# Optimization experiments

Hardware: AMD Instinct MI355X
Metric: run time of the kernel (lower is better)

## Reference

```python
import jax, jax.numpy as jnp
from jax import lax
import numpy as np


def setup_inputs() -> dict:
    key = jax.random.key(0)
    kx, = jax.random.split(key, 1)
    B, T = 4096, 4096
    x = jax.random.normal(kx, (B, T), dtype=jnp.float32)
    omega_log = jnp.asarray(0.0, dtype=jnp.float32)
    alpha_log = jnp.asarray(0.0, dtype=jnp.float32)
    beta_log = jnp.asarray(0.0, dtype=jnp.float32)
    return {"x": x, "omega_log": omega_log, "alpha_log": alpha_log, "beta_log": beta_log}


def reference(x, omega_log, alpha_log, beta_log):
    # x: [B, T]
    ea = jnp.exp(alpha_log)
    eb = jnp.exp(beta_log)
    denom = 1.0 + ea + eb
    omega = jnp.exp(omega_log)
    alpha = ea / denom
    beta = eb / denom

    # initial variance: unbiased sample variance over time (torch.var default ddof=1)
    s0 = jnp.var(x, axis=1, ddof=1)  # [B]

    xsq = jnp.swapaxes(x[:, :-1] ** 2, 0, 1)  # [T-1, B]

    def step(s_prev, x2_t):
        s_t = omega + alpha * x2_t + beta * s_prev
        return s_t, s_t

    _, rest = lax.scan(step, s0, xsq)  # rest: [T-1, B]
    sigma2 = jnp.concatenate([s0[None, :], rest], axis=0)  # [T, B]
    return jnp.sqrt(jnp.swapaxes(sigma2, 0, 1))  # [B, T]
```

## Files before the change

kernel.cpp:

```cpp
#include <hip/hip_runtime.h>
#include <math.h>

#define B_ROWS 4096
#define T_COLS 4096
#define NTHREADS 256
#define CHUNK 16
#define NWAVES (NTHREADS / 64)

__device__ __forceinline__ int paddr(int e) { return e + (e >> 4); }
#define LDS_FLOATS (T_COLS + (T_COLS >> 4))

__global__ __launch_bounds__(NTHREADS) void garch_fused(
    const float* __restrict__ x,
    const float* __restrict__ p_omega_log,
    const float* __restrict__ p_alpha_log,
    const float* __restrict__ p_beta_log,
    float* __restrict__ out)
{
    __shared__ float lds[LDS_FLOATS];
    __shared__ float wA[NWAVES], wB[NWAVES];
    __shared__ float rSum[NWAVES], rSsq[NWAVES];

    const int t    = threadIdx.x;
    const int lane = t & 63;
    const int wv   = t >> 6;
    const int row  = blockIdx.x;
    const long rbase = (long)row * T_COLS;

    float ea = expf(p_alpha_log[0]);
    float eb = expf(p_beta_log[0]);
    float denom = 1.0f + ea + eb;
    float omega = expf(p_omega_log[0]);
    float alpha = ea / denom;
    float beta  = eb / denom;
    float b2 = beta * beta, b4 = b2 * b2, b8 = b4 * b4, b16 = b8 * b8;

    const float4* xv = reinterpret_cast<const float4*>(x + rbase);
#pragma unroll
    for (int k = 0; k < 4; ++k) {
        int e4 = k * 1024 + 4 * t;
        float4 v = xv[k * 256 + t];
        int a0 = paddr(e4);
        lds[a0 + 0] = v.x; lds[a0 + 1] = v.y; lds[a0 + 2] = v.z; lds[a0 + 3] = v.w;
    }
    __syncthreads();

    float xr[CHUNK];
    int cbase = 17 * t;
#pragma unroll
    for (int i = 0; i < CHUNK; ++i) xr[i] = lds[cbase + i];
    float prev = (t > 0) ? lds[paddr(CHUNK * t - 1)] : 0.0f;

    float sum = 0.0f, ssq = 0.0f;
#pragma unroll
    for (int i = 0; i < CHUNK; ++i) { sum += xr[i]; ssq = fmaf(xr[i], xr[i], ssq); }

    float bpart = 0.0f;
    if (t > 0) bpart = fmaf(alpha, prev * prev, omega);
#pragma unroll
    for (int i = 0; i < CHUNK - 1; ++i)
        bpart = fmaf(beta, bpart, fmaf(alpha, xr[i] * xr[i], omega));
    float apart = (t == 0) ? (b8 * b4 * b2 * beta) : b16;

    float s1 = sum, s2 = ssq;
#pragma unroll
    for (int d = 32; d > 0; d >>= 1) {
        s1 += __shfl_xor(s1, d);
        s2 += __shfl_xor(s2, d);
    }
    if (lane == 0) { rSum[wv] = s1; rSsq[wv] = s2; }
    __syncthreads();
    float tsum = rSum[0] + rSum[1] + rSum[2] + rSum[3];
    float tssq = rSsq[0] + rSsq[1] + rSsq[2] + rSsq[3];
    float s0 = (tssq - tsum * tsum * (1.0f / T_COLS)) * (1.0f / (T_COLS - 1));
    s0 = fmaxf(s0, 0.0f);

    float ia = apart, ib = bpart;
#pragma unroll
    for (int d = 1; d < 64; d <<= 1) {
        float pa = __shfl_up(ia, d);
        float pb = __shfl_up(ib, d);
        if (lane >= d) { ib = fmaf(ia, pb, ib); ia = ia * pa; }
    }
    if (lane == 63) { wA[wv] = ia; wB[wv] = ib; }
    __syncthreads();
    float sw = s0;
#pragma unroll
    for (int w = 0; w < NWAVES - 1; ++w)
        if (w < wv) sw = fmaf(wA[w], sw, wB[w]);
    float ea_ = __shfl_up(ia, 1);
    float eb_ = __shfl_up(ib, 1);
    if (lane == 0) { ea_ = 1.0f; eb_ = 0.0f; }
    float s = fmaf(ea_, sw, eb_);

    if (t == 0) {
        lds[cbase] = sqrtf(s);
#pragma unroll
        for (int i = 0; i < CHUNK - 1; ++i) {
            s = fmaf(beta, s, fmaf(alpha, xr[i] * xr[i], omega));
            lds[cbase + 1 + i] = sqrtf(s);
        }
    } else {
        s = fmaf(beta, s, fmaf(alpha, prev * prev, omega));
        lds[cbase] = sqrtf(s);
#pragma unroll
        for (int i = 0; i < CHUNK - 1; ++i) {
            s = fmaf(beta, s, fmaf(alpha, xr[i] * xr[i], omega));
            lds[cbase + 1 + i] = sqrtf(s);
        }
    }
    __syncthreads();

    float4* ov = reinterpret_cast<float4*>(out + rbase);
#pragma unroll
    for (int k = 0; k < 4; ++k) {
        int e4 = k * 1024 + 4 * t;
        int a0 = paddr(e4);
        float4 v;
        v.x = lds[a0 + 0]; v.y = lds[a0 + 1]; v.z = lds[a0 + 2]; v.w = lds[a0 + 3];
        ov[k * 256 + t] = v;
    }
}

extern "C" void kernel_launch(void* const* d_in, const int* in_sizes, int n_in,
                              void* d_out, int out_size, void* d_ws, size_t ws_size,
                              hipStream_t stream) {
    const float* x         = (const float*)d_in[0];
    const float* omega_log = (const float*)d_in[1];
    const float* alpha_log = (const float*)d_in[2];
    const float* beta_log  = (const float*)d_in[3];
    float* out = (float*)d_out;

    garch_fused<<<B_ROWS, NTHREADS, 0, stream>>>(x, omega_log, alpha_log, beta_log, out);
}
```

Measured before the change: 115.5 us.

## Load and store row chunks directly per thread, dropping LDS staging

Each thread now loads its 16 contiguous elements straight from global memory as four float4s and writes its outputs the same way, removing the LDS transpose buffer and two block barriers. The neighbouring element comes from a wave shuffle, with a scalar global load at wave boundaries. The two reductions now share one barrier, and sqrt uses the hardware builtin. The cost is strided per-thread accesses (64 bytes per thread per row chunk), which coalesce less cleanly than the original lane-contiguous float4 pattern.

```diff
diff --git a/kernel.cpp b/kernel.cpp
--- a/kernel.cpp
+++ b/kernel.cpp
@@ -7,9 +7,6 @@
 #define CHUNK 16
 #define NWAVES (NTHREADS / 64)
 
-__device__ __forceinline__ int paddr(int e) { return e + (e >> 4); }
-#define LDS_FLOATS (T_COLS + (T_COLS >> 4))
-
 __global__ __launch_bounds__(NTHREADS) void garch_fused(
     const float* __restrict__ x,
     const float* __restrict__ p_omega_log,
@@ -17,15 +14,12 @@
     const float* __restrict__ p_beta_log,
     float* __restrict__ out)
 {
-    __shared__ float lds[LDS_FLOATS];
-    __shared__ float wA[NWAVES], wB[NWAVES];
-    __shared__ float rSum[NWAVES], rSsq[NWAVES];
+    __shared__ float wA[NWAVES], wB[NWAVES], rSum[NWAVES], rSsq[NWAVES];
 
     const int t    = threadIdx.x;
     const int lane = t & 63;
     const int wv   = t >> 6;
-    const int row  = blockIdx.x;
-    const long rbase = (long)row * T_COLS;
+    const long rbase = (long)blockIdx.x * T_COLS;
 
     float ea = expf(p_alpha_log[0]);
     float eb = expf(p_beta_log[0]);
@@ -35,21 +29,13 @@
     float beta  = eb / denom;
     float b2 = beta * beta, b4 = b2 * b2, b8 = b4 * b4, b16 = b8 * b8;
 
-    const float4* xv = reinterpret_cast<const float4*>(x + rbase);
-#pragma unroll
-    for (int k = 0; k < 4; ++k) {
-        int e4 = k * 1024 + 4 * t;
-        float4 v = xv[k * 256 + t];
-        int a0 = paddr(e4);
-        lds[a0 + 0] = v.x; lds[a0 + 1] = v.y; lds[a0 + 2] = v.z; lds[a0 + 3] = v.w;
-    }
-    __syncthreads();
+    const float4* xv = reinterpret_cast<const float4*>(x + rbase + (long)CHUNK * t);
+    float4 v0 = xv[0], v1 = xv[1], v2 = xv[2], v3 = xv[3];
+    float xr[CHUNK] = { v0.x, v0.y, v0.z, v0.w,  v1.x, v1.y, v1.z, v1.w,
+                        v2.x, v2.y, v2.z, v2.w,  v3.x, v3.y, v3.z, v3.w };
 
-    float xr[CHUNK];
-    int cbase = 17 * t;
-#pragma unroll
-    for (int i = 0; i < CHUNK; ++i) xr[i] = lds[cbase + i];
-    float prev = (t > 0) ? lds[paddr(CHUNK * t - 1)] : 0.0f;
+    float prev = __shfl_up(xr[CHUNK - 1], 1);
+    if (lane == 0) prev = (t > 0) ? x[rbase + (long)CHUNK * t - 1] : 0.0f;
 
     float sum = 0.0f, ssq = 0.0f;
 #pragma unroll
@@ -68,12 +54,6 @@
         s1 += __shfl_xor(s1, d);
         s2 += __shfl_xor(s2, d);
     }
-    if (lane == 0) { rSum[wv] = s1; rSsq[wv] = s2; }
-    __syncthreads();
-    float tsum = rSum[0] + rSum[1] + rSum[2] + rSum[3];
-    float tssq = rSsq[0] + rSsq[1] + rSsq[2] + rSsq[3];
-    float s0 = (tssq - tsum * tsum * (1.0f / T_COLS)) * (1.0f / (T_COLS - 1));
-    s0 = fmaxf(s0, 0.0f);
 
     float ia = apart, ib = bpart;
 #pragma unroll
@@ -82,44 +62,49 @@
         float pb = __shfl_up(ib, d);
         if (lane >= d) { ib = fmaf(ia, pb, ib); ia = ia * pa; }
     }
-    if (lane == 63) { wA[wv] = ia; wB[wv] = ib; }
+
+    if (lane == 0)  { rSum[wv] = s1; rSsq[wv] = s2; }
+    if (lane == 63) { wA[wv] = ia;   wB[wv] = ib;  }
     __syncthreads();
+
+    float tsum = rSum[0] + rSum[1] + rSum[2] + rSum[3];
+    float tssq = rSsq[0] + rSsq[1] + rSsq[2] + rSsq[3];
+    float s0 = (tssq - tsum * tsum * (1.0f / T_COLS)) * (1.0f / (T_COLS - 1));
+    s0 = fmaxf(s0, 0.0f);
+
     float sw = s0;
 #pragma unroll
     for (int w = 0; w < NWAVES - 1; ++w)
         if (w < wv) sw = fmaf(wA[w], sw, wB[w]);
+
     float ea_ = __shfl_up(ia, 1);
     float eb_ = __shfl_up(ib, 1);
     if (lane == 0) { ea_ = 1.0f; eb_ = 0.0f; }
     float s = fmaf(ea_, sw, eb_);
 
+    float o[CHUNK];
     if (t == 0) {
-        lds[cbase] = sqrtf(s);
+        o[0] = __builtin_amdgcn_sqrtf(s);
 #pragma unroll
         for (int i = 0; i < CHUNK - 1; ++i) {
             s = fmaf(beta, s, fmaf(alpha, xr[i] * xr[i], omega));
-            lds[cbase + 1 + i] = sqrtf(s);
+            o[1 + i] = __builtin_amdgcn_sqrtf(s);
         }
     } else {
         s = fmaf(beta, s, fmaf(alpha, prev * prev, omega));
-        lds[cbase] = sqrtf(s);
+        o[0] = __builtin_amdgcn_sqrtf(s);
 #pragma unroll
         for (int i = 0; i < CHUNK - 1; ++i) {
             s = fmaf(beta, s, fmaf(alpha, xr[i] * xr[i], omega));
-            lds[cbase + 1 + i] = sqrtf(s);
+            o[1 + i] = __builtin_amdgcn_sqrtf(s);
         }
     }
-    __syncthreads();
 
-    float4* ov = reinterpret_cast<float4*>(out + rbase);
-#pragma unroll
-    for (int k = 0; k < 4; ++k) {
-        int e4 = k * 1024 + 4 * t;
-        int a0 = paddr(e4);
-        float4 v;
-        v.x = lds[a0 + 0]; v.y = lds[a0 + 1]; v.z = lds[a0 + 2]; v.w = lds[a0 + 3];
-        ov[k * 256 + t] = v;
-    }
+    float4* ov = reinterpret_cast<float4*>(out + rbase + (long)CHUNK * t);
+    ov[0] = make_float4(o[0],  o[1],  o[2],  o[3]);
+    ov[1] = make_float4(o[4],  o[5],  o[6],  o[7]);
+    ov[2] = make_float4(o[8],  o[9],  o[10], o[11]);
+    ov[3] = make_float4(o[12], o[13], o[14], o[15]);
 }
 
 extern "C" void kernel_launch(void* const* d_in, const int* in_sizes, int n_in,
```

New measurement: 123.4 us. 1.07x slower.
